# Kernel tuning notes

Measured on AMD Instinct MI355X. Metric: run time of the kernel, lower is better.

Reference implementation:

```python
import jax, jax.numpy as jnp
import numpy as np
import math

DIM = 512
NUM_HEADS = 8
DIM_HEAD = DIM // NUM_HEADS


def normalized_coords(h, w):
    # (h*w, 2) with (x, y) in [0, 1]
    y = jnp.linspace(0.0, 1.0, h)
    x = jnp.linspace(0.0, 1.0, w)
    yg, xg = jnp.meshgrid(y, x, indexing='ij')
    return jnp.stack([xg.ravel(), yg.ravel()], axis=-1)


def rotate_half(x):
    dh = x.shape[-1] // 2
    return jnp.concatenate([-x[..., dh:], x[..., :dh]], axis=-1)


def apply_rope(t, coords):
    # t: (n, heads, seq, dim_head); coords: (seq, 2) (identical across batch)
    dim_half = t.shape[-1] // 2
    freq = 1.0 / (10000.0 ** (jnp.arange(dim_half, dtype=jnp.float32) / dim_half))
    ang_x = coords[:, 0:1] * freq  # (seq, dim_half)
    ang_y = coords[:, 1:2] * freq
    ang = jnp.concatenate([ang_x, ang_y], axis=-1)  # (seq, dim_head)
    cos, sin = jnp.cos(ang), jnp.sin(ang)
    return t * cos + rotate_half(t) * sin


def setup_inputs() -> dict:
    key = jax.random.key(0)
    ks = jax.random.split(key, 12)
    n, Np, d, H, W = 4, 1024, DIM, 64, 64
    s = 0.02
    return {
        'local_feat': jax.random.normal(ks[0], (n, Np, d), jnp.float32),
        'global_feat': jax.random.normal(ks[1], (n, d, H, W), jnp.float32),
        'Wq': jax.random.normal(ks[2], (d, d), jnp.float32) * s,
        'bq': jnp.zeros((d,), jnp.float32),
        'Wk': jax.random.normal(ks[3], (d, d), jnp.float32) * s,
        'bk': jnp.zeros((d,), jnp.float32),
        'Wv': jax.random.normal(ks[4], (d, d), jnp.float32) * s,
        'bv': jnp.zeros((d,), jnp.float32),
        'Wg': jax.random.normal(ks[5], (d, 2 * d), jnp.float32) * s,
        'bg': jnp.zeros((d,), jnp.float32),
        'Wo': jax.random.normal(ks[6], (d, d), jnp.float32) * s,
        'bo': jnp.zeros((d,), jnp.float32),
    }


def reference(local_feat, global_feat, Wq, bq, Wk, bk, Wv, bv, Wg, bg, Wo, bo):
    n, Np, d = local_feat.shape
    _, _, H, W = global_feat.shape
    h, dh = NUM_HEADS, DIM_HEAD
    gf = global_feat.reshape(n, d, H * W).transpose(0, 2, 1)  # (n, HW, d)

    P = int(math.isqrt(Np))
    local_coords = normalized_coords(P, P)      # (Np, 2)
    global_coords = normalized_coords(H, W)     # (HW, 2)

    def proj(x, Wt, b):
        return x @ Wt.T + b

    Q = proj(local_feat, Wq, bq).reshape(n, Np, h, dh).transpose(0, 2, 1, 3)
    K = proj(gf, Wk, bk).reshape(n, H * W, h, dh).transpose(0, 2, 1, 3)
    V = proj(gf, Wv, bv).reshape(n, H * W, h, dh).transpose(0, 2, 1, 3)

    Q = apply_rope(Q, local_coords)
    K = apply_rope(K, global_coords)

    scores = jnp.einsum('bhqd,bhkd->bhqk', Q, K) / math.sqrt(dh)
    attn = jax.nn.softmax(scores, axis=-1)
    ao = jnp.einsum('bhqk,bhkd->bhqd', attn, V)
    ao = ao.transpose(0, 2, 1, 3).reshape(n, Np, d)

    gate = jax.nn.sigmoid(jnp.concatenate([local_feat, ao], axis=-1) @ Wg.T + bg)
    enhanced = local_feat + gate * ao
    return enhanced @ Wo.T + bo
```

## Files before the change

kernel.cpp:

```cpp
#include <hip/hip_runtime.h>
#include <hip/hip_bf16.h>
#include <cstdint>

typedef __hip_bfloat16 BF;
typedef unsigned short ushort_t;
typedef __attribute__((ext_vector_type(8))) __bf16 bf16x8;
typedef __attribute__((ext_vector_type(4))) float f32x4;
typedef __attribute__((ext_vector_type(4))) unsigned uint4v;

__device__ __forceinline__ float bu2f(ushort_t u) {
  return __uint_as_float((unsigned)u << 16);
}
__device__ __forceinline__ unsigned pk2(float a, float b) {
  union { __hip_bfloat162 h; unsigned u; } c;
  c.h = __float22bfloat162_rn(make_float2(a, b));
  return c.u;
}
__device__ __forceinline__ unsigned short f2bu(float f) {
  union { BF b; unsigned short u; } c; c.b = __float2bfloat16(f); return c.u;
}
__device__ __forceinline__ float b2f(BF x) { return __bfloat162float(x); }
__device__ __forceinline__ void rd16f(const float* fp, ushort_t* out) {
#pragma unroll
  for (int j = 0; j < 16; j += 4) {
    float4 v = *(const float4*)(fp + j);
    ((unsigned*)out)[j / 2] = pk2(v.x, v.y);
    ((unsigned*)out)[j / 2 + 1] = pk2(v.z, v.w);
  }
}

#define QS 0.1803368801111f

__global__ __launch_bounds__(256) void pre_k(const float* __restrict__ local,
                                             const float* __restrict__ gfeat,
                                             const float* __restrict__ Wq,
                                             const float* __restrict__ bq,
                                             const float* __restrict__ Wk,
                                             const float* __restrict__ Wv,
                                             const float* __restrict__ Wg,
                                             const float* __restrict__ Wo,
                                             BF* __restrict__ gfT,
                                             BF* __restrict__ Qb,
                                             BF* __restrict__ localB,
                                             BF* __restrict__ WB) {
  __shared__ __align__(16) ushort_t smem[2][64][72];
  const int t = threadIdx.x;
  if (blockIdx.x >= 2560) {
    if (WB) {
      size_t e = ((size_t)(blockIdx.x - 2560) * 256 + t) * 16;
      const float* src;
      BF* dst;
      if (e < 2097152) {
        src = local + e;  dst = localB + e;
      } else {
        size_t f = e - 2097152;
        dst = WB + f;
        if (f < 262144)        src = Wq + f;
        else if (f < 524288)   src = Wk + (f - 262144);
        else if (f < 786432)   src = Wv + (f - 524288);
        else if (f < 1310720)  src = Wg + (f - 786432);
        else                   src = Wo + (f - 1310720);
      }
      ushort_t vals[16];
      rd16f(src, vals);
      *(uint4*)dst = *(uint4*)&vals[0];
      *((uint4*)dst + 1) = *(uint4*)&vals[8];
    }
    return;
  }
  if (blockIdx.x < 2048) {
    auto T = smem[0];
    const int g = blockIdx.x;
    const int bz = g & 3, mt = (g >> 2) & 63, kt = g >> 8;
    {
      int krow = t >> 2, mg = t & 3;
      ushort_t vals[16];
      rd16f(gfeat + (size_t)bz * 512 * 4096 + (size_t)(kt * 64 + krow) * 4096 +
                mt * 64 + mg * 16,
            vals);
#pragma unroll
      for (int j = 0; j < 16; ++j) T[mg * 16 + j][krow] = vals[j];
    }
    __syncthreads();
    int mrow = t >> 2, kg = t & 3;
    uint4 a = *(const uint4*)&T[mrow][kg * 16];
    uint4 b = *(const uint4*)&T[mrow][kg * 16 + 8];
    size_t o = ((size_t)bz * 4096 + mt * 64 + mrow) * 512 + kt * 64 + kg * 16;
    *(uint4*)&gfT[o] = a;
    *(uint4*)&gfT[o + 8] = b;
    return;
  }
  auto As = smem[0];
  auto Bs = smem[1];
  const int bx = blockIdx.x - 2048;
  const int m0 = (bx & 63) * 64, n0 = (bx >> 6) * 64;
  const int w = t >> 6, lane = t & 63;
  const int quad = lane >> 4, l16 = lane & 15;

  f32x4 acc[4] = {};
  for (int k0 = 0; k0 < 512; k0 += 64) {
    __syncthreads();
    {
      int row = t >> 2, cg = t & 3;
      int kg = k0 + cg * 16;
      ushort_t vals[16];
      rd16f(local + (size_t)(m0 + row) * 512 + kg, vals);
      *(uint4*)&As[row][cg * 16] = *(uint4*)&vals[0];
      *(uint4*)&As[row][cg * 16 + 8] = *(uint4*)&vals[8];
      ushort_t bv[16];
      rd16f(Wq + (size_t)(n0 + row) * 512 + kg, bv);
      *(uint4*)&Bs[row][cg * 16] = *(uint4*)&bv[0];
      *(uint4*)&Bs[row][cg * 16 + 8] = *(uint4*)&bv[8];
    }
    __syncthreads();
#pragma unroll
    for (int kc = 0; kc < 2; ++kc) {
      bf16x8 af = *(const bf16x8*)&As[w * 16 + l16][kc * 32 + quad * 8];
#pragma unroll
      for (int nt = 0; nt < 4; ++nt) {
        bf16x8 bfv = *(const bf16x8*)&Bs[nt * 16 + l16][kc * 32 + quad * 8];
        acc[nt] = __builtin_amdgcn_mfma_f32_16x16x32_bf16(af, bfv, acc[nt], 0, 0, 0);
      }
    }
  }
  const int head = n0 >> 6;
#pragma unroll
  for (int r = 0; r < 4; ++r) {
    int mg = m0 + w * 16 + quad * 4 + r;
    int bb = mg >> 10, qi = mg & 1023;
    float x = (float)(qi & 31) * (1.f / 31.f);
    float y = (float)(qi >> 5) * (1.f / 31.f);
    size_t base = (((size_t)bb * 8 + head) * 1024 + qi) * 64;
#pragma unroll
    for (int j = 0; j < 2; ++j) {
      int c0 = j * 16 + l16;
      float t0 = acc[j][r] + bq[head * 64 + c0];
      float t1 = acc[j + 2][r] + bq[head * 64 + c0 + 32];
      float fr = __expf((float)c0 * (-9.210340371976184f / 32.f));
      float ax = x * fr, ay = y * fr;
      Qb[base + c0] = __float2bfloat16((t0 * __cosf(ax) - t1 * __sinf(ax)) * QS);
      Qb[base + c0 + 32] = __float2bfloat16((t1 * __cosf(ay) + t0 * __sinf(ay)) * QS);
    }
  }
}

__global__ __launch_bounds__(256) void kv_k(const BF* __restrict__ gfT,
                                            const float* __restrict__ Wk,
                                            const float* __restrict__ Wv,
                                            const BF* __restrict__ WkB,
                                            const BF* __restrict__ WvB,
                                            const float* __restrict__ bk,
                                            const float* __restrict__ bv,
                                            BF* __restrict__ Kb,
                                            BF* __restrict__ VTb) {
  __shared__ __align__(16) ushort_t smem[2][128][72];
  auto As = smem[0];
  auto Bs = smem[1];
  const int tid = threadIdx.x;
  const int w = tid >> 6, lane = tid & 63;
  const int quad = lane >> 4, l16 = lane & 15;
  const int wm = w >> 1, wn = w & 1;
  const int g = blockIdx.x;
  const int a = g & 7, y = (g >> 3) & 7, bidx = g >> 6;
  const int m0 = ((bidx << 1) | (a & 1)) * 128;
  const int n0 = y * 128;
  const int bz = a >> 1;

  f32x4 acc[4][4] = {};
  for (int k0 = 0; k0 < 512; k0 += 64) {
    __syncthreads();
#pragma unroll
    for (int u = 0; u < 2; ++u) {
      int unit = tid + u * 256;
      int row = unit >> 2, cg = unit & 3;
      const uint4* p = (const uint4*)(gfT + ((size_t)bz * 4096 + m0 + row) * 512 +
                                      k0 + cg * 16);
      *(uint4*)&As[row][cg * 16] = p[0];
      *(uint4*)&As[row][cg * 16 + 8] = p[1];
    }
    if (WkB) {
      const BF* bb16 = (n0 >= 512) ? WvB : WkB;
      const int nb = (n0 >= 512) ? (n0 - 512) : n0;
#pragma unroll
      for (int u = 0; u < 2; ++u) {
        int unit = tid + u * 256;
        int row = unit >> 2, cg = unit & 3;
        const uint4* p = (const uint4*)(bb16 + (size_t)(nb + row) * 512 +
                                        k0 + cg * 16);
        *(uint4*)&Bs[row][cg * 16] = p[0];
        *(uint4*)&Bs[row][cg * 16 + 8] = p[1];
      }
    } else {
#pragma unroll
      for (int u = 0; u < 2; ++u) {
        int unit = tid + u * 256;
        int row = unit >> 2, cg = unit & 3;
        const float* bsrc = (n0 >= 512) ? Wv : Wk;
        size_t nrow = (n0 >= 512) ? (n0 - 512 + row) : (n0 + row);
        ushort_t vals[16];
        rd16f(bsrc + nrow * 512 + k0 + cg * 16, vals);
        *(uint4*)&Bs[row][cg * 16] = *(uint4*)&vals[0];
        *(uint4*)&Bs[row][cg * 16 + 8] = *(uint4*)&vals[8];
      }
    }
    __syncthreads();
#pragma unroll
    for (int kc = 0; kc < 2; ++kc) {
      bf16x8 af[4], bfv[4];
#pragma unroll
      for (int i = 0; i < 4; ++i) {
        af[i] = *(const bf16x8*)&As[wm * 64 + i * 16 + l16][kc * 32 + quad * 8];
        bfv[i] = *(const bf16x8*)&Bs[wn * 64 + i * 16 + l16][kc * 32 + quad * 8];
      }
#pragma unroll
      for (int mt = 0; mt < 4; ++mt)
#pragma unroll
        for (int nt = 0; nt < 4; ++nt)
          acc[mt][nt] = __builtin_amdgcn_mfma_f32_16x16x32_bf16(af[mt], bfv[nt], acc[mt][nt], 0, 0, 0);
    }
  }
  if (n0 < 512) {
    const int head = (n0 + wn * 64) >> 6;
#pragma unroll
    for (int mt = 0; mt < 4; ++mt)
#pragma unroll
      for (int r = 0; r < 4; ++r) {
        int pg = m0 + wm * 64 + mt * 16 + quad * 4 + r;
        float x = (float)(pg & 63) * (1.f / 63.f);
        float yy = (float)(pg >> 6) * (1.f / 63.f);
        size_t base = (((size_t)bz * 8 + head) * 4096 + pg) * 64;
#pragma unroll
        for (int j = 0; j < 2; ++j) {
          int c0 = j * 16 + l16;
          float t0 = acc[mt][j][r] + bk[head * 64 + c0];
          float t1 = acc[mt][j + 2][r] + bk[head * 64 + c0 + 32];
          float fr = __expf((float)c0 * (-9.210340371976184f / 32.f));
          float ax = x * fr, ay = yy * fr;
          Kb[base + c0] = __float2bfloat16(t0 * __cosf(ax) - t1 * __sinf(ax));
          Kb[base + c0 + 32] = __float2bfloat16(t1 * __cosf(ay) + t0 * __sinf(ay));
        }
      }
  } else {
    const int n0v = n0 - 512;
    __syncthreads();
    ushort_t (*T)[136] = (ushort_t(*)[136]) & smem[0][0][0];
#pragma unroll
    for (int mt = 0; mt < 4; ++mt)
#pragma unroll
      for (int nt = 0; nt < 4; ++nt)
#pragma unroll
        for (int r = 0; r < 4; ++r) {
          int n_l = wn * 64 + nt * 16 + l16;
          int m_l = wm * 64 + mt * 16 + quad * 4 + r;
          T[n_l][m_l] = f2bu(acc[mt][nt][r] + bv[n0v + n_l]);
        }
    __syncthreads();
    int row = tid >> 1, half = tid & 1;
    size_t gbase = (((size_t)bz * 8 + (n0v >> 6) + (row >> 6)) * 64 + (row & 63)) * 4096 +
                   m0 + half * 64;
    uint4* dst = (uint4*)(VTb + gbase);
    const uint4* src = (const uint4*)&T[row][half * 64];
#pragma unroll
    for (int j = 0; j < 8; ++j) dst[j] = src[j];
  }
}

template <int NS>
__global__ __launch_bounds__(256, 4) void attn_k(const BF* __restrict__ Q,
                                                 const BF* __restrict__ K,
                                                 const BF* __restrict__ VT,
                                                 BF* __restrict__ AO,
                                                 BF* __restrict__ Opart,
                                                 float* __restrict__ lpart) {
  __shared__ __align__(16) ushort_t Ks[2][64][64];
  __shared__ __align__(16) ushort_t VTs[3][64][64];

  const int tid = threadIdx.x;
  const int w = tid >> 6, lane = tid & 63;
  const int quad = lane >> 4, l16 = lane & 15;
  const int r3 = l16 & 7;
  const int sc0 = (quad ^ r3) << 3;
  const int sc1 = sc0 ^ 32;

  const int g = blockIdx.x;
  const int bh = g & 31;
  const int qt = (g >> 5) & 7;
  const int ks = g >> 8;
  const int b = bh >> 3, h = bh & 7;
  const int q0 = qt * 128 + w * 32;
  const int kspan = 4096 / NS, kbase = ks * kspan;

  bf16x8 qa[2][2];
#pragma unroll
  for (int qs = 0; qs < 2; ++qs) {
    const BF* qp = Q + (((size_t)bh << 10) + q0 + qs * 16 + l16) * 64 + quad * 8;
    qa[qs][0] = *(const bf16x8*)qp;
    qa[qs][1] = *(const bf16x8*)(qp + 32);
  }
  bf16x8 ones;
#pragma unroll
  for (int j = 0; j < 8; ++j) ones[j] = (__bf16)1.0f;

  const BF* Kp = K + (size_t)bh * 4096 * 64;
  const BF* VTp = VT + (size_t)bh * 64 * 4096;

  f32x4 o[2][4] = {};
  f32x4 ol[2] = {};

  const int srow = tid >> 2, scol = (tid & 3) * 16;
  const int ssc = ((2 * (tid & 3)) ^ (srow & 7)) << 3;
  int vcol[4];
  {
    const int s1 = (tid >> 1) & 1, s0v = tid & 1;
#pragma unroll
    for (int gq = 0; gq < 4; ++gq)
      vcol[gq] = (((s1 * 4 + gq) ^ (srow & 7)) << 3) + s0v * 4;
  }

#define STAGE_V(buf, v0, v1)                                   \
  {                                                            \
    uint2 t_;                                                  \
    t_.x = (v0).x; t_.y = (v0).y; *(uint2*)&VTs[buf][srow][vcol[0]] = t_; \
    t_.x = (v0).z; t_.y = (v0).w; *(uint2*)&VTs[buf][srow][vcol[1]] = t_; \
    t_.x = (v1).x; t_.y = (v1).y; *(uint2*)&VTs[buf][srow][vcol[2]] = t_; \
    t_.x = (v1).z; t_.y = (v1).w; *(uint2*)&VTs[buf][srow][vcol[3]] = t_; \
  }

  {
    const uint4* kp = (const uint4*)(Kp + (size_t)(kbase + srow) * 64 + scol);
    const uint4* vp = (const uint4*)(VTp + (size_t)srow * 4096 + kbase + scol);
    uint4 a = kp[0], bb = kp[1], c = vp[0], d = vp[1];
    *(uint4*)&Ks[0][srow][ssc] = a;  *(uint4*)&Ks[0][srow][ssc ^ 8] = bb;
    STAGE_V(0, c, d);
  }
  __syncthreads();

  bf16x8 pa[2][2];

#define S_PHASE(KRD)                                                          \
  {                                                                           \
    unsigned pu[2][2][4];                                                     \
    _Pragma("unroll") for (int ct = 0; ct < 4; ++ct) {                        \
      const int krow = ct * 16 + l16;                                         \
      bf16x8 kb0 = *(const bf16x8*)&Ks[KRD][krow][sc0];                       \
      bf16x8 kb1 = *(const bf16x8*)&Ks[KRD][krow][sc1];                       \
      _Pragma("unroll") for (int qs = 0; qs < 2; ++qs) {                      \
        f32x4 s = {};                                                         \
        s = __builtin_amdgcn_mfma_f32_16x16x32_bf16(kb0, qa[qs][0], s, 0, 0, 0); \
        s = __builtin_amdgcn_mfma_f32_16x16x32_bf16(kb1, qa[qs][1], s, 0, 0, 0); \
        pu[qs][ct >> 1][(ct & 1) * 2] =                                       \
            pk2(__builtin_exp2f(s[0]), __builtin_exp2f(s[1]));                \
        pu[qs][ct >> 1][(ct & 1) * 2 + 1] =                                   \
            pk2(__builtin_exp2f(s[2]), __builtin_exp2f(s[3]));                \
      }                                                                       \
    }                                                                         \
    _Pragma("unroll") for (int qs = 0; qs < 2; ++qs)                          \
      _Pragma("unroll") for (int kk = 0; kk < 2; ++kk) {                      \
        uint4v u = {pu[qs][kk][0], pu[qs][kk][1], pu[qs][kk][2],              \
                    pu[qs][kk][3]};                                           \
        pa[qs][kk] = __builtin_bit_cast(bf16x8, u);                           \
      }                                                                       \
  }

#define PV_PHASE(VRD)                                                         \
  {                                                                           \
    _Pragma("unroll") for (int qs = 0; qs < 2; ++qs) {                        \
      ol[qs] = __builtin_amdgcn_mfma_f32_16x16x32_bf16(ones, pa[qs][0], ol[qs], 0, 0, 0); \
      ol[qs] = __builtin_amdgcn_mfma_f32_16x16x32_bf16(ones, pa[qs][1], ol[qs], 0, 0, 0); \
    }                                                                         \
    _Pragma("unroll") for (int nt = 0; nt < 4; ++nt) {                        \
      const int vrow = nt * 16 + l16;                                         \
      bf16x8 vb0 = *(const bf16x8*)&VTs[VRD][vrow][sc0];                      \
      bf16x8 vb1 = *(const bf16x8*)&VTs[VRD][vrow][sc1];                      \
      _Pragma("unroll") for (int qs = 0; qs < 2; ++qs) {                      \
        o[qs][nt] = __builtin_amdgcn_mfma_f32_16x16x32_bf16(vb0, pa[qs][0], o[qs][nt], 0, 0, 0); \
        o[qs][nt] = __builtin_amdgcn_mfma_f32_16x16x32_bf16(vb1, pa[qs][1], o[qs][nt], 0, 0, 0); \
      }                                                                       \
    }                                                                         \
  }

  const int nc = kspan / 64;
  {
    uint4 nk0, nk1, nv0, nv1;
    const bool more = (nc > 1);
    if (more) {
      const int c1 = kbase + 64;
      const uint4* kp = (const uint4*)(Kp + (size_t)(c1 + srow) * 64 + scol);
      const uint4* vp = (const uint4*)(VTp + (size_t)srow * 4096 + c1 + scol);
      nk0 = kp[0]; nk1 = kp[1]; nv0 = vp[0]; nv1 = vp[1];
    }
    __builtin_amdgcn_s_setprio(1);
    S_PHASE(0);
    __builtin_amdgcn_s_setprio(0);
    if (more) {
      *(uint4*)&Ks[1][srow][ssc] = nk0;
      *(uint4*)&Ks[1][srow][ssc ^ 8] = nk1;
      STAGE_V(1, nv0, nv1);
    }
    __syncthreads();
  }

  int krd = 1, vrd = 0, vwr = 2;
  for (int c = 1; c < nc; ++c) {
    uint4 nk0, nk1, nv0, nv1;
    const bool more = (c + 1 < nc);
    if (more) {
      const int c1 = kbase + (c + 1) * 64;
      const uint4* kp = (const uint4*)(Kp + (size_t)(c1 + srow) * 64 + scol);
      const uint4* vp = (const uint4*)(VTp + (size_t)srow * 4096 + c1 + scol);
      nk0 = kp[0]; nk1 = kp[1]; nv0 = vp[0]; nv1 = vp[1];
    }
    __builtin_amdgcn_s_setprio(1);
    PV_PHASE(vrd);
    S_PHASE(krd);
    __builtin_amdgcn_s_setprio(0);
    if (more) {
      *(uint4*)&Ks[krd ^ 1][srow][ssc] = nk0;
      *(uint4*)&Ks[krd ^ 1][srow][ssc ^ 8] = nk1;
      STAGE_V(vwr, nv0, nv1);
    }
    __syncthreads();
    krd ^= 1;
    vrd = (vrd == 2) ? 0 : vrd + 1;
    vwr = (vwr == 2) ? 0 : vwr + 1;
  }
  PV_PHASE(vrd);
#undef STAGE_V
#undef S_PHASE
#undef PV_PHASE

#pragma unroll
  for (int qs = 0; qs < 2; ++qs) {
    int qg = q0 + qs * 16 + l16;
    if (NS == 1) {
      float invl = 1.f / ol[qs][0];
#pragma unroll
      for (int nt = 0; nt < 4; ++nt) {
        uint2 uu;
        uu.x = pk2(o[qs][nt][0] * invl, o[qs][nt][1] * invl);
        uu.y = pk2(o[qs][nt][2] * invl, o[qs][nt][3] * invl);
        *(uint2*)(AO + (((size_t)b << 10) + qg) * 512 + h * 64 + nt * 16 + quad * 4) = uu;
      }
    } else {
      if (quad == 0) lpart[ks * 32768 + (bh << 10) + qg] = ol[qs][0];
#pragma unroll
      for (int nt = 0; nt < 4; ++nt) {
        uint2 uu;
        uu.x = pk2(o[qs][nt][0], o[qs][nt][1]);
        uu.y = pk2(o[qs][nt][2], o[qs][nt][3]);
        *(uint2*)(Opart + (size_t)ks * 2097152 + (((size_t)bh << 10) + qg) * 64 +
                  nt * 16 + quad * 4) = uu;
      }
    }
  }
}

template <int NS>
__global__ __launch_bounds__(256) void gate_k(const float* __restrict__ local,
                                              const BF* __restrict__ localB,
                                              const BF* __restrict__ AO,
                                              const BF* __restrict__ Opart,
                                              const float* __restrict__ lpart,
                                              const float* __restrict__ Wg,
                                              const BF* __restrict__ WgB,
                                              const float* __restrict__ bg,
                                              BF* __restrict__ ENH) {
  __shared__ __align__(16) ushort_t As[64][72];
  __shared__ __align__(16) ushort_t Bs[64][72];
  const int tid = threadIdx.x;
  const int w = tid >> 6, lane = tid & 63;
  const int quad = lane >> 4, l16 = lane & 15;
  const int m0 = blockIdx.x * 64, n0 = blockIdx.y * 64;

  f32x4 acc[4] = {};
  float aosv[4][4];
  for (int k0 = 0; k0 < 1024; k0 += 64) {
    __syncthreads();
    {
      int row = tid >> 2, cg = tid & 3;
      int kg = k0 + cg * 16;
      ushort_t vals[16];
      if (kg < 512) {
        if (localB) {
          const uint4* p = (const uint4*)(localB + (size_t)(m0 + row) * 512 + kg);
          *(uint4*)&vals[0] = p[0]; *(uint4*)&vals[8] = p[1];
        } else {
          rd16f(local + (size_t)(m0 + row) * 512 + kg, vals);
        }
      } else {
        int c = kg - 512;
        int hh = c >> 6, dh0 = c & 63;
        int mg = m0 + row;
        size_t bq = (size_t)(((mg >> 10) * 8 + hh) << 10) + (mg & 1023);
        if (NS == 1) {
          const uint4* p = (const uint4*)(AO + (size_t)mg * 512 + c);
          *(uint4*)&vals[0] = p[0]; *(uint4*)&vals[8] = p[1];
        } else {
          float ls = 0.f;
#pragma unroll
          for (int s2 = 0; s2 < NS; ++s2) ls += lpart[s2 * 32768 + bq];
          float inv = 1.f / ls;
          float av[16] = {};
#pragma unroll
          for (int s2 = 0; s2 < NS; ++s2) {
            const ushort_t* op = (const ushort_t*)Opart + (size_t)s2 * 2097152 +
                                 bq * 64 + dh0;
            uint4 u0 = ((const uint4*)op)[0], u1 = ((const uint4*)op)[1];
            const ushort_t* pu = (const ushort_t*)&u0;
#pragma unroll
            for (int j = 0; j < 8; ++j) av[j] += bu2f(pu[j]);
            pu = (const ushort_t*)&u1;
#pragma unroll
            for (int j = 0; j < 8; ++j) av[8 + j] += bu2f(pu[j]);
          }
#pragma unroll
          for (int j = 0; j < 16; j += 2)
            ((unsigned*)vals)[j / 2] = pk2(av[j] * inv, av[j + 1] * inv);
        }
      }
      *(uint4*)&As[row][cg * 16] = *(uint4*)&vals[0];
      *(uint4*)&As[row][cg * 16 + 8] = *(uint4*)&vals[8];
      if (WgB) {
        const uint4* p = (const uint4*)(WgB + (size_t)(n0 + row) * 1024 + kg);
        *(uint4*)&Bs[row][cg * 16] = p[0];
        *(uint4*)&Bs[row][cg * 16 + 8] = p[1];
      } else {
        ushort_t bv[16];
        rd16f(Wg + (size_t)(n0 + row) * 1024 + kg, bv);
        *(uint4*)&Bs[row][cg * 16] = *(uint4*)&bv[0];
        *(uint4*)&Bs[row][cg * 16 + 8] = *(uint4*)&bv[8];
      }
    }
    __syncthreads();
    if (k0 == 512 + n0) {
#pragma unroll
      for (int r = 0; r < 4; ++r)
#pragma unroll
        for (int nt = 0; nt < 4; ++nt)
          aosv[r][nt] = bu2f(As[w * 16 + quad * 4 + r][nt * 16 + l16]);
    }
#pragma unroll
    for (int kc = 0; kc < 2; ++kc) {
      bf16x8 af = *(const bf16x8*)&As[w * 16 + l16][kc * 32 + quad * 8];
#pragma unroll
      for (int nt = 0; nt < 4; ++nt) {
        bf16x8 bfv = *(const bf16x8*)&Bs[nt * 16 + l16][kc * 32 + quad * 8];
        acc[nt] = __builtin_amdgcn_mfma_f32_16x16x32_bf16(af, bfv, acc[nt], 0, 0, 0);
      }
    }
  }
#pragma unroll
  for (int r = 0; r < 4; ++r) {
    int mg = m0 + w * 16 + quad * 4 + r;
#pragma unroll
    for (int nt = 0; nt < 4; ++nt) {
      int ng = n0 + nt * 16 + l16;
      size_t idx = (size_t)mg * 512 + ng;
      float gg = 1.f / (1.f + __expf(-(acc[nt][r] + bg[ng])));
      ENH[idx] = __float2bfloat16(local[idx] + gg * aosv[r][nt]);
    }
  }
}

__global__ __launch_bounds__(256) void out_k(const BF* __restrict__ ENH,
                                             const float* __restrict__ Wo,
                                             const BF* __restrict__ WoB,
                                             const float* __restrict__ bo,
                                             float* __restrict__ out) {
  __shared__ __align__(16) ushort_t As[64][72];
  __shared__ __align__(16) ushort_t Bs[64][72];
  const int tid = threadIdx.x;
  const int w = tid >> 6, lane = tid & 63;
  const int quad = lane >> 4, l16 = lane & 15;
  const int m0 = blockIdx.x * 64, n0 = blockIdx.y * 64;

  f32x4 acc[4] = {};
  for (int k0 = 0; k0 < 512; k0 += 64) {
    __syncthreads();
    {
      int row = tid >> 2, cg = tid & 3;
      int kg = k0 + cg * 16;
      const uint4* p = (const uint4*)(ENH + (size_t)(m0 + row) * 512 + kg);
      *(uint4*)&As[row][cg * 16] = p[0];
      *(uint4*)&As[row][cg * 16 + 8] = p[1];
      if (WoB) {
        const uint4* pb = (const uint4*)(WoB + (size_t)(n0 + row) * 512 + kg);
        *(uint4*)&Bs[row][cg * 16] = pb[0];
        *(uint4*)&Bs[row][cg * 16 + 8] = pb[1];
      } else {
        ushort_t bv[16];
        rd16f(Wo + (size_t)(n0 + row) * 512 + kg, bv);
        *(uint4*)&Bs[row][cg * 16] = *(uint4*)&bv[0];
        *(uint4*)&Bs[row][cg * 16 + 8] = *(uint4*)&bv[8];
      }
    }
    __syncthreads();
#pragma unroll
    for (int kc = 0; kc < 2; ++kc) {
      bf16x8 af = *(const bf16x8*)&As[w * 16 + l16][kc * 32 + quad * 8];
#pragma unroll
      for (int nt = 0; nt < 4; ++nt) {
        bf16x8 bfv = *(const bf16x8*)&Bs[nt * 16 + l16][kc * 32 + quad * 8];
        acc[nt] = __builtin_amdgcn_mfma_f32_16x16x32_bf16(af, bfv, acc[nt], 0, 0, 0);
      }
    }
  }
#pragma unroll
  for (int r = 0; r < 4; ++r) {
    int mg = m0 + w * 16 + quad * 4 + r;
#pragma unroll
    for (int nt = 0; nt < 4; ++nt) {
      int ng = n0 + nt * 16 + l16;
      out[(size_t)mg * 512 + ng] = acc[nt][r] + bo[ng];
    }
  }
}

extern "C" void kernel_launch(void* const* d_in, const int* in_sizes, int n_in,
                              void* d_out, int out_size, void* d_ws, size_t ws_size,
                              hipStream_t stream) {
  const float* local = (const float*)d_in[0];
  const float* gfeat = (const float*)d_in[1];
  const float* Wq = (const float*)d_in[2];
  const float* bq = (const float*)d_in[3];
  const float* Wk = (const float*)d_in[4];
  const float* bk = (const float*)d_in[5];
  const float* Wv = (const float*)d_in[6];
  const float* bv = (const float*)d_in[7];
  const float* Wg = (const float*)d_in[8];
  const float* bg = (const float*)d_in[9];
  const float* Wo = (const float*)d_in[10];
  const float* bo = (const float*)d_in[11];

  char* w = (char*)d_ws;
  BF* Qb = (BF*)w;            w += (size_t)2097152 * 2;
  BF* Kb = (BF*)w;            w += (size_t)8388608 * 2;
  BF* VTb = (BF*)w;           w += (size_t)8388608 * 2;
  BF* AO = (BF*)w;            w += (size_t)2097152 * 2;
  BF* gfT = (BF*)w;
  BF* Opart = (BF*)w;
  size_t baseOff = (size_t)(w - (char*)d_ws);
  BF* ENH = Qb;

  int NS = 1;
  if (baseOff + 4 * (4194304 + 131072) <= ws_size) NS = 4;
  else if (baseOff + 16777216 + 2 * 131072 <= ws_size) NS = 2;
  float* lpart = (float*)(w + (size_t)NS * 4194304);

  size_t xsize = (size_t)NS * (4194304 + 131072);
  if (xsize < 16777216) xsize = 16777216;
  BF* WB = (BF*)(w + xsize);
  BF* localB = WB + 1572864;
  bool useP = (baseOff + xsize + 3145728 + 4194304) <= ws_size;
  const BF *WkB = nullptr, *WvB = nullptr, *WgB = nullptr, *WoB = nullptr,
           *locB = nullptr;
  BF *WBo = nullptr, *localBo = nullptr;
  if (useP) {
    WBo = WB;  localBo = localB;
    WkB = WB + 262144;  WvB = WB + 524288;
    WgB = WB + 786432;  WoB = WB + 1310720;  locB = localB;
  }

  dim3 blk(256);
  pre_k<<<dim3(useP ? 3456 : 2560), blk, 0, stream>>>(
      local, gfeat, Wq, bq, Wk, Wv, Wg, Wo, gfT, Qb, localBo, WBo);
  kv_k<<<dim3(1024), blk, 0, stream>>>(gfT, Wk, Wv, WkB, WvB, bk, bv, Kb, VTb);
  if (NS == 4) {
    attn_k<4><<<dim3(1024), blk, 0, stream>>>(Qb, Kb, VTb, AO, Opart, lpart);
    gate_k<4><<<dim3(64, 8), blk, 0, stream>>>(local, locB, AO, Opart, lpart, Wg, WgB, bg, ENH);
  } else if (NS == 2) {
    attn_k<2><<<dim3(512), blk, 0, stream>>>(Qb, Kb, VTb, AO, Opart, lpart);
    gate_k<2><<<dim3(64, 8), blk, 0, stream>>>(local, locB, AO, Opart, lpart, Wg, WgB, bg, ENH);
  } else {
    attn_k<1><<<dim3(256), blk, 0, stream>>>(Qb, Kb, VTb, AO, nullptr, nullptr);
    gate_k<1><<<dim3(64, 8), blk, 0, stream>>>(local, locB, AO, Opart, lpart, Wg, WgB, bg, ENH);
  }
  out_k<<<dim3(64, 8), blk, 0, stream>>>(ENH, Wo, WoB, bo, (float*)d_out);
}
```

Baseline: 241.0 us.

## Prefetch next K-tile into registers in kv, gate and output GEMM kernels

```diff
diff --git a/kernel.cpp b/kernel.cpp
--- a/kernel.cpp
+++ b/kernel.cpp
@@ -144,15 +144,15 @@
   }
 }
 
-__global__ __launch_bounds__(256) void kv_k(const BF* __restrict__ gfT,
-                                            const float* __restrict__ Wk,
-                                            const float* __restrict__ Wv,
-                                            const BF* __restrict__ WkB,
-                                            const BF* __restrict__ WvB,
-                                            const float* __restrict__ bk,
-                                            const float* __restrict__ bv,
-                                            BF* __restrict__ Kb,
-                                            BF* __restrict__ VTb) {
+__global__ __launch_bounds__(256, 2) void kv_k(const BF* __restrict__ gfT,
+                                               const float* __restrict__ Wk,
+                                               const float* __restrict__ Wv,
+                                               const BF* __restrict__ WkB,
+                                               const BF* __restrict__ WvB,
+                                               const float* __restrict__ bk,
+                                               const float* __restrict__ bv,
+                                               BF* __restrict__ Kb,
+                                               BF* __restrict__ VTb) {
   __shared__ __align__(16) ushort_t smem[2][128][72];
   auto As = smem[0];
   auto Bs = smem[1];
@@ -167,30 +167,63 @@
   const int bz = a >> 1;
 
   f32x4 acc[4][4] = {};
-  for (int k0 = 0; k0 < 512; k0 += 64) {
-    __syncthreads();
-#pragma unroll
-    for (int u = 0; u < 2; ++u) {
-      int unit = tid + u * 256;
-      int row = unit >> 2, cg = unit & 3;
-      const uint4* p = (const uint4*)(gfT + ((size_t)bz * 4096 + m0 + row) * 512 +
-                                      k0 + cg * 16);
-      *(uint4*)&As[row][cg * 16] = p[0];
-      *(uint4*)&As[row][cg * 16 + 8] = p[1];
-    }
-    if (WkB) {
-      const BF* bb16 = (n0 >= 512) ? WvB : WkB;
-      const int nb = (n0 >= 512) ? (n0 - 512) : n0;
+  if (WkB) {
+    const BF* bb16 = (n0 >= 512) ? WvB : WkB;
+    const int nb = (n0 >= 512) ? (n0 - 512) : n0;
+    uint4 ra[2][2], rb[2][2];
+#define KV_LOAD(K0)                                                          \
+    _Pragma("unroll") for (int u = 0; u < 2; ++u) {                          \
+      int unit = tid + u * 256;                                              \
+      int row = unit >> 2, cg = unit & 3;                                    \
+      const uint4* pA = (const uint4*)(gfT + ((size_t)bz * 4096 + m0 + row) * \
+                                       512 + (K0) + cg * 16);                \
+      ra[u][0] = pA[0]; ra[u][1] = pA[1];                                    \
+      const uint4* pB = (const uint4*)(bb16 + (size_t)(nb + row) * 512 +     \
+                                       (K0) + cg * 16);                      \
+      rb[u][0] = pB[0]; rb[u][1] = pB[1];                                    \
+    }
+    KV_LOAD(0);
+    for (int k0 = 0; k0 < 512; k0 += 64) {
+      __syncthreads();
 #pragma unroll
       for (int u = 0; u < 2; ++u) {
         int unit = tid + u * 256;
         int row = unit >> 2, cg = unit & 3;
-        const uint4* p = (const uint4*)(bb16 + (size_t)(nb + row) * 512 +
+        *(uint4*)&As[row][cg * 16] = ra[u][0];
+        *(uint4*)&As[row][cg * 16 + 8] = ra[u][1];
+        *(uint4*)&Bs[row][cg * 16] = rb[u][0];
+        *(uint4*)&Bs[row][cg * 16 + 8] = rb[u][1];
+      }
+      __syncthreads();
+      if (k0 + 64 < 512) { KV_LOAD(k0 + 64); }
+#pragma unroll
+      for (int kc = 0; kc < 2; ++kc) {
+        bf16x8 af[4], bfv[4];
+#pragma unroll
+        for (int i = 0; i < 4; ++i) {
+          af[i] = *(const bf16x8*)&As[wm * 64 + i * 16 + l16][kc * 32 + quad * 8];
+          bfv[i] = *(const bf16x8*)&Bs[wn * 64 + i * 16 + l16][kc * 32 + quad * 8];
+        }
+#pragma unroll
+        for (int mt = 0; mt < 4; ++mt)
+#pragma unroll
+          for (int nt = 0; nt < 4; ++nt)
+            acc[mt][nt] = __builtin_amdgcn_mfma_f32_16x16x32_bf16(af[mt], bfv[nt], acc[mt][nt], 0, 0, 0);
+      }
+    }
+#undef KV_LOAD
+  } else {
+    for (int k0 = 0; k0 < 512; k0 += 64) {
+      __syncthreads();
+#pragma unroll
+      for (int u = 0; u < 2; ++u) {
+        int unit = tid + u * 256;
+        int row = unit >> 2, cg = unit & 3;
+        const uint4* p = (const uint4*)(gfT + ((size_t)bz * 4096 + m0 + row) * 512 +
                                         k0 + cg * 16);
-        *(uint4*)&Bs[row][cg * 16] = p[0];
-        *(uint4*)&Bs[row][cg * 16 + 8] = p[1];
-      }
-    } else {
+        *(uint4*)&As[row][cg * 16] = p[0];
+        *(uint4*)&As[row][cg * 16 + 8] = p[1];
+      }
 #pragma unroll
       for (int u = 0; u < 2; ++u) {
         int unit = tid + u * 256;
@@ -202,21 +235,21 @@
         *(uint4*)&Bs[row][cg * 16] = *(uint4*)&vals[0];
         *(uint4*)&Bs[row][cg * 16 + 8] = *(uint4*)&vals[8];
       }
-    }
-    __syncthreads();
-#pragma unroll
-    for (int kc = 0; kc < 2; ++kc) {
-      bf16x8 af[4], bfv[4];
-#pragma unroll
-      for (int i = 0; i < 4; ++i) {
-        af[i] = *(const bf16x8*)&As[wm * 64 + i * 16 + l16][kc * 32 + quad * 8];
-        bfv[i] = *(const bf16x8*)&Bs[wn * 64 + i * 16 + l16][kc * 32 + quad * 8];
-      }
-#pragma unroll
-      for (int mt = 0; mt < 4; ++mt)
-#pragma unroll
-        for (int nt = 0; nt < 4; ++nt)
-          acc[mt][nt] = __builtin_amdgcn_mfma_f32_16x16x32_bf16(af[mt], bfv[nt], acc[mt][nt], 0, 0, 0);
+      __syncthreads();
+#pragma unroll
+      for (int kc = 0; kc < 2; ++kc) {
+        bf16x8 af[4], bfv[4];
+#pragma unroll
+        for (int i = 0; i < 4; ++i) {
+          af[i] = *(const bf16x8*)&As[wm * 64 + i * 16 + l16][kc * 32 + quad * 8];
+          bfv[i] = *(const bf16x8*)&Bs[wn * 64 + i * 16 + l16][kc * 32 + quad * 8];
+        }
+#pragma unroll
+        for (int mt = 0; mt < 4; ++mt)
+#pragma unroll
+          for (int nt = 0; nt < 4; ++nt)
+            acc[mt][nt] = __builtin_amdgcn_mfma_f32_16x16x32_bf16(af[mt], bfv[nt], acc[mt][nt], 0, 0, 0);
+      }
     }
   }
   if (n0 < 512) {
@@ -456,60 +489,76 @@
 }
 
 template <int NS>
-__global__ __launch_bounds__(256) void gate_k(const float* __restrict__ local,
-                                              const BF* __restrict__ localB,
-                                              const BF* __restrict__ AO,
-                                              const BF* __restrict__ Opart,
-                                              const float* __restrict__ lpart,
-                                              const float* __restrict__ Wg,
-                                              const BF* __restrict__ WgB,
-                                              const float* __restrict__ bg,
-                                              BF* __restrict__ ENH) {
+__global__ __launch_bounds__(256, 2) void gate_k(const float* __restrict__ local,
+                                                 const BF* __restrict__ localB,
+                                                 const BF* __restrict__ AO,
+                                                 const BF* __restrict__ Opart,
+                                                 const float* __restrict__ lpart,
+                                                 const float* __restrict__ Wg,
+                                                 const BF* __restrict__ WgB,
+                                                 const float* __restrict__ bg,
+                                                 BF* __restrict__ ENH) {
   __shared__ __align__(16) ushort_t As[64][72];
   __shared__ __align__(16) ushort_t Bs[64][72];
   const int tid = threadIdx.x;
   const int w = tid >> 6, lane = tid & 63;
   const int quad = lane >> 4, l16 = lane & 15;
   const int m0 = blockIdx.x * 64, n0 = blockIdx.y * 64;
+  const int srow = tid >> 2, scg = tid & 3;
 
   f32x4 acc[4] = {};
   float aosv[4][4];
-  for (int k0 = 0; k0 < 1024; k0 += 64) {
-    __syncthreads();
-    {
-      int row = tid >> 2, cg = tid & 3;
-      int kg = k0 + cg * 16;
-      ushort_t vals[16];
-      if (kg < 512) {
-        if (localB) {
-          const uint4* p = (const uint4*)(localB + (size_t)(m0 + row) * 512 + kg);
-          *(uint4*)&vals[0] = p[0]; *(uint4*)&vals[8] = p[1];
-        } else {
-          rd16f(local + (size_t)(m0 + row) * 512 + kg, vals);
-        }
-      } else {
-        int c = kg - 512;
-        int hh = c >> 6, dh0 = c & 63;
-        int mg = m0 + row;
-        size_t bq = (size_t)(((mg >> 10) * 8 + hh) << 10) + (mg & 1023);
-        if (NS == 1) {
-          const uint4* p = (const uint4*)(AO + (size_t)mg * 512 + c);
-          *(uint4*)&vals[0] = p[0]; *(uint4*)&vals[8] = p[1];
+
+  if (localB && WgB) {
+    uint4 rA[2], rB[2];
+    uint4 rO[NS][2];
+    float rl[NS];
+#define GT_LOAD(K0)                                                           \
+    {                                                                         \
+      int kg = (K0) + scg * 16;                                               \
+      const uint4* pb = (const uint4*)(WgB + (size_t)(n0 + srow) * 1024 + kg);\
+      rB[0] = pb[0]; rB[1] = pb[1];                                           \
+      if (kg < 512) {                                                         \
+        const uint4* p = (const uint4*)(localB + (size_t)(m0 + srow) * 512 + kg); \
+        rA[0] = p[0]; rA[1] = p[1];                                           \
+      } else {                                                                \
+        int c = kg - 512;                                                     \
+        int hh = c >> 6, dh0 = c & 63;                                        \
+        int mg = m0 + srow;                                                   \
+        size_t bq = (size_t)(((mg >> 10) * 8 + hh) << 10) + (mg & 1023);      \
+        if (NS == 1) {                                                        \
+          const uint4* p = (const uint4*)(AO + (size_t)mg * 512 + c);         \
+          rA[0] = p[0]; rA[1] = p[1];                                         \
+        } else {                                                              \
+          _Pragma("unroll") for (int s2 = 0; s2 < NS; ++s2) {                 \
+            rl[s2] = lpart[s2 * 32768 + bq];                                  \
+            const uint4* op = (const uint4*)((const ushort_t*)Opart +         \
+                              (size_t)s2 * 2097152 + bq * 64 + dh0);          \
+            rO[s2][0] = op[0]; rO[s2][1] = op[1];                             \
+          }                                                                   \
+        }                                                                     \
+      }                                                                       \
+    }
+    GT_LOAD(0);
+    for (int k0 = 0; k0 < 1024; k0 += 64) {
+      __syncthreads();
+      {
+        int kg = k0 + scg * 16;
+        ushort_t vals[16];
+        if (kg < 512 || NS == 1) {
+          *(uint4*)&vals[0] = rA[0]; *(uint4*)&vals[8] = rA[1];
         } else {
           float ls = 0.f;
 #pragma unroll
-          for (int s2 = 0; s2 < NS; ++s2) ls += lpart[s2 * 32768 + bq];
+          for (int s2 = 0; s2 < NS; ++s2) ls += rl[s2];
           float inv = 1.f / ls;
           float av[16] = {};
 #pragma unroll
           for (int s2 = 0; s2 < NS; ++s2) {
-            const ushort_t* op = (const ushort_t*)Opart + (size_t)s2 * 2097152 +
-                                 bq * 64 + dh0;
-            uint4 u0 = ((const uint4*)op)[0], u1 = ((const uint4*)op)[1];
-            const ushort_t* pu = (const ushort_t*)&u0;
+            const ushort_t* pu = (const ushort_t*)&rO[s2][0];
 #pragma unroll
             for (int j = 0; j < 8; ++j) av[j] += bu2f(pu[j]);
-            pu = (const ushort_t*)&u1;
+            pu = (const ushort_t*)&rO[s2][1];
 #pragma unroll
             for (int j = 0; j < 8; ++j) av[8 + j] += bu2f(pu[j]);
           }
@@ -517,35 +566,94 @@
           for (int j = 0; j < 16; j += 2)
             ((unsigned*)vals)[j / 2] = pk2(av[j] * inv, av[j + 1] * inv);
         }
-      }
-      *(uint4*)&As[row][cg * 16] = *(uint4*)&vals[0];
-      *(uint4*)&As[row][cg * 16 + 8] = *(uint4*)&vals[8];
-      if (WgB) {
-        const uint4* p = (const uint4*)(WgB + (size_t)(n0 + row) * 1024 + kg);
-        *(uint4*)&Bs[row][cg * 16] = p[0];
-        *(uint4*)&Bs[row][cg * 16 + 8] = p[1];
-      } else {
+        *(uint4*)&As[srow][scg * 16] = *(uint4*)&vals[0];
+        *(uint4*)&As[srow][scg * 16 + 8] = *(uint4*)&vals[8];
+        *(uint4*)&Bs[srow][scg * 16] = rB[0];
+        *(uint4*)&Bs[srow][scg * 16 + 8] = rB[1];
+      }
+      __syncthreads();
+      if (k0 + 64 < 1024) { GT_LOAD(k0 + 64); }
+      if (k0 == 512 + n0) {
+#pragma unroll
+        for (int r = 0; r < 4; ++r)
+#pragma unroll
+          for (int nt = 0; nt < 4; ++nt)
+            aosv[r][nt] = bu2f(As[w * 16 + quad * 4 + r][nt * 16 + l16]);
+      }
+#pragma unroll
+      for (int kc = 0; kc < 2; ++kc) {
+        bf16x8 af = *(const bf16x8*)&As[w * 16 + l16][kc * 32 + quad * 8];
+#pragma unroll
+        for (int nt = 0; nt < 4; ++nt) {
+          bf16x8 bfv = *(const bf16x8*)&Bs[nt * 16 + l16][kc * 32 + quad * 8];
+          acc[nt] = __builtin_amdgcn_mfma_f32_16x16x32_bf16(af, bfv, acc[nt], 0, 0, 0);
+        }
+      }
+    }
+#undef GT_LOAD
+  } else {
+    for (int k0 = 0; k0 < 1024; k0 += 64) {
+      __syncthreads();
+      {
+        int row = srow, cg = scg;
+        int kg = k0 + cg * 16;
+        ushort_t vals[16];
+        if (kg < 512) {
+          rd16f(local + (size_t)(m0 + row) * 512 + kg, vals);
+        } else {
+          int c = kg - 512;
+          int hh = c >> 6, dh0 = c & 63;
+          int mg = m0 + row;
+          size_t bq = (size_t)(((mg >> 10) * 8 + hh) << 10) + (mg & 1023);
+          if (NS == 1) {
+            const uint4* p = (const uint4*)(AO + (size_t)mg * 512 + c);
+            *(uint4*)&vals[0] = p[0]; *(uint4*)&vals[8] = p[1];
+          } else {
+            float ls = 0.f;
+#pragma unroll
+            for (int s2 = 0; s2 < NS; ++s2) ls += lpart[s2 * 32768 + bq];
+            float inv = 1.f / ls;
+            float av[16] = {};
+#pragma unroll
+            for (int s2 = 0; s2 < NS; ++s2) {
+              const ushort_t* op = (const ushort_t*)Opart + (size_t)s2 * 2097152 +
+                                   bq * 64 + dh0;
+              uint4 u0 = ((const uint4*)op)[0], u1 = ((const uint4*)op)[1];
+              const ushort_t* pu = (const ushort_t*)&u0;
+#pragma unroll
+              for (int j = 0; j < 8; ++j) av[j] += bu2f(pu[j]);
+              pu = (const ushort_t*)&u1;
+#pragma unroll
+              for (int j = 0; j < 8; ++j) av[8 + j] += bu2f(pu[j]);
+            }
+#pragma unroll
+            for (int j = 0; j < 16; j += 2)
+              ((unsigned*)vals)[j / 2] = pk2(av[j] * inv, av[j + 1] * inv);
+          }
+        }
+        *(uint4*)&As[row][cg * 16] = *(uint4*)&vals[0];
+        *(uint4*)&As[row][cg * 16 + 8] = *(uint4*)&vals[8];
         ushort_t bv[16];
         rd16f(Wg + (size_t)(n0 + row) * 1024 + kg, bv);
         *(uint4*)&Bs[row][cg * 16] = *(uint4*)&bv[0];
         *(uint4*)&Bs[row][cg * 16 + 8] = *(uint4*)&bv[8];
       }
-    }
-    __syncthreads();
-    if (k0 == 512 + n0) {
-#pragma unroll
-      for (int r = 0; r < 4; ++r)
-#pragma unroll
-        for (int nt = 0; nt < 4; ++nt)
-          aosv[r][nt] = bu2f(As[w * 16 + quad * 4 + r][nt * 16 + l16]);
-    }
-#pragma unroll
-    for (int kc = 0; kc < 2; ++kc) {
-      bf16x8 af = *(const bf16x8*)&As[w * 16 + l16][kc * 32 + quad * 8];
-#pragma unroll
-      for (int nt = 0; nt < 4; ++nt) {
-        bf16x8 bfv = *(const bf16x8*)&Bs[nt * 16 + l16][kc * 32 + quad * 8];
-        acc[nt] = __builtin_amdgcn_mfma_f32_16x16x32_bf16(af, bfv, acc[nt], 0, 0, 0);
+      __syncthreads();
+      if (k0 == 512 + n0) {
+#pragma unroll
+        for (int r = 0; r < 4; ++r)
+#pragma unroll
+          for (int nt = 0; nt < 4; ++nt)
+            aosv[r][nt] = bu2f(As[w * 16 + quad * 4 + r][nt * 16 + l16]);
+      }
+#pragma unroll
+      for (int kc = 0; kc < 2; ++kc) {
+        bf16x8 af = *(const bf16x8*)&As[w * 16 + l16][kc * 32 + quad * 8];
+#pragma unroll
+        for (int nt = 0; nt < 4; ++nt) {
+          bf16x8 bfv = *(const bf16x8*)&Bs[nt * 16 + l16][kc * 32 + quad * 8];
+          acc[nt] = __builtin_amdgcn_mfma_f32_16x16x32_bf16(af, bfv, acc[nt], 0, 0, 0);
+        }
       }
     }
   }
@@ -562,46 +670,72 @@
   }
 }
 
-__global__ __launch_bounds__(256) void out_k(const BF* __restrict__ ENH,
-                                             const float* __restrict__ Wo,
-                                             const BF* __restrict__ WoB,
-                                             const float* __restrict__ bo,
-                                             float* __restrict__ out) {
+__global__ __launch_bounds__(256, 2) void out_k(const BF* __restrict__ ENH,
+                                                const float* __restrict__ Wo,
+                                                const BF* __restrict__ WoB,
+                                                const float* __restrict__ bo,
+                                                float* __restrict__ out) {
   __shared__ __align__(16) ushort_t As[64][72];
   __shared__ __align__(16) ushort_t Bs[64][72];
   const int tid = threadIdx.x;
   const int w = tid >> 6, lane = tid & 63;
   const int quad = lane >> 4, l16 = lane & 15;
   const int m0 = blockIdx.x * 64, n0 = blockIdx.y * 64;
+  const int srow = tid >> 2, scg = tid & 3;
 
   f32x4 acc[4] = {};
-  for (int k0 = 0; k0 < 512; k0 += 64) {
-    __syncthreads();
-    {
-      int row = tid >> 2, cg = tid & 3;
-      int kg = k0 + cg * 16;
-      const uint4* p = (const uint4*)(ENH + (size_t)(m0 + row) * 512 + kg);
-      *(uint4*)&As[row][cg * 16] = p[0];
-      *(uint4*)&As[row][cg * 16 + 8] = p[1];
-      if (WoB) {
-        const uint4* pb = (const uint4*)(WoB + (size_t)(n0 + row) * 512 + kg);
-        *(uint4*)&Bs[row][cg * 16] = pb[0];
-        *(uint4*)&Bs[row][cg * 16 + 8] = pb[1];
-      } else {
+  if (WoB) {
+    uint4 rA[2], rB[2];
+#define OT_LOAD(K0)                                                           \
+    {                                                                         \
+      const uint4* pa = (const uint4*)(ENH + (size_t)(m0 + srow) * 512 +      \
+                                       (K0) + scg * 16);                      \
+      rA[0] = pa[0]; rA[1] = pa[1];                                           \
+      const uint4* pb = (const uint4*)(WoB + (size_t)(n0 + srow) * 512 +      \
+                                       (K0) + scg * 16);                      \
+      rB[0] = pb[0]; rB[1] = pb[1];                                           \
+    }
+    OT_LOAD(0);
+    for (int k0 = 0; k0 < 512; k0 += 64) {
+      __syncthreads();
+      *(uint4*)&As[srow][scg * 16] = rA[0];
+      *(uint4*)&As[srow][scg * 16 + 8] = rA[1];
+      *(uint4*)&Bs[srow][scg * 16] = rB[0];
+      *(uint4*)&Bs[srow][scg * 16 + 8] = rB[1];
+      __syncthreads();
+      if (k0 + 64 < 512) { OT_LOAD(k0 + 64); }
+#pragma unroll
+      for (int kc = 0; kc < 2; ++kc) {
+        bf16x8 af = *(const bf16x8*)&As[w * 16 + l16][kc * 32 + quad * 8];
+#pragma unroll
+        for (int nt = 0; nt < 4; ++nt) {
+          bf16x8 bfv = *(const bf16x8*)&Bs[nt * 16 + l16][kc * 32 + quad * 8];
+          acc[nt] = __builtin_amdgcn_mfma_f32_16x16x32_bf16(af, bfv, acc[nt], 0, 0, 0);
+        }
+      }
+    }
+#undef OT_LOAD
+  } else {
+    for (int k0 = 0; k0 < 512; k0 += 64) {
+      __syncthreads();
+      {
+        const uint4* p = (const uint4*)(ENH + (size_t)(m0 + srow) * 512 + k0 + scg * 16);
+        *(uint4*)&As[srow][scg * 16] = p[0];
+        *(uint4*)&As[srow][scg * 16 + 8] = p[1];
         ushort_t bv[16];
-        rd16f(Wo + (size_t)(n0 + row) * 512 + kg, bv);
-        *(uint4*)&Bs[row][cg * 16] = *(uint4*)&bv[0];
-        *(uint4*)&Bs[row][cg * 16 + 8] = *(uint4*)&bv[8];
-      }
-    }
-    __syncthreads();
-#pragma unroll
-    for (int kc = 0; kc < 2; ++kc) {
-      bf16x8 af = *(const bf16x8*)&As[w * 16 + l16][kc * 32 + quad * 8];
-#pragma unroll
-      for (int nt = 0; nt < 4; ++nt) {
-        bf16x8 bfv = *(const bf16x8*)&Bs[nt * 16 + l16][kc * 32 + quad * 8];
-        acc[nt] = __builtin_amdgcn_mfma_f32_16x16x32_bf16(af, bfv, acc[nt], 0, 0, 0);
+        rd16f(Wo + (size_t)(n0 + srow) * 512 + k0 + scg * 16, bv);
+        *(uint4*)&Bs[srow][scg * 16] = *(uint4*)&bv[0];
+        *(uint4*)&Bs[srow][scg * 16 + 8] = *(uint4*)&bv[8];
+      }
+      __syncthreads();
+#pragma unroll
+      for (int kc = 0; kc < 2; ++kc) {
+        bf16x8 af = *(const bf16x8*)&As[w * 16 + l16][kc * 32 + quad * 8];
+#pragma unroll
+        for (int nt = 0; nt < 4; ++nt) {
+          bf16x8 bfv = *(const bf16x8*)&Bs[nt * 16 + l16][kc * 32 + quad * 8];
+          acc[nt] = __builtin_amdgcn_mfma_f32_16x16x32_bf16(af, bfv, acc[nt], 0, 0, 0);
+        }
       }
     }
   }
```

New measurement: 317.5 us. 31.8% more time.
